# Kernel tuning notes

Measured on AMD Instinct MI355X. Metric: run time of the kernel, lower is better.

## Reference

```python
import jax, jax.numpy as jnp
import numpy as np

N = 100000        # nodes
E = 1_600_000     # edges (before self loops)
G = 512           # graphs in batch
IN = 64           # in_channels
HID = 48          # hidden_channels
H = 4             # heads
C = HID // H      # per-head channels
OUT = 10          # out_channels


def setup_inputs() -> dict:
    key = jax.random.key(0)
    ks = jax.random.split(key, 24)
    s = 0.1
    inp = {
        "x": jax.random.normal(ks[0], (N, IN), jnp.float32),
        "edge_index": jax.random.randint(ks[1], (2, E), 0, N, dtype=jnp.int64),
        "edge_weight": jax.random.uniform(ks[2], (E,), jnp.float32),
        "batch": jnp.sort(jax.random.randint(ks[3], (N,), 0, G, dtype=jnp.int64)),
        # GATConv layer 0 (IN -> H*C), layers 1,2 (HID -> H*C); bias=False
        "Wg0": jax.random.normal(ks[4], (IN, HID), jnp.float32) * s,
        "as0": jax.random.normal(ks[5], (H, C), jnp.float32) * s,
        "ad0": jax.random.normal(ks[6], (H, C), jnp.float32) * s,
        "Wg1": jax.random.normal(ks[7], (HID, HID), jnp.float32) * s,
        "as1": jax.random.normal(ks[8], (H, C), jnp.float32) * s,
        "ad1": jax.random.normal(ks[9], (H, C), jnp.float32) * s,
        "Wg2": jax.random.normal(ks[10], (HID, HID), jnp.float32) * s,
        "as2": jax.random.normal(ks[11], (H, C), jnp.float32) * s,
        "ad2": jax.random.normal(ks[12], (H, C), jnp.float32) * s,
        # MLP head: Linear(HID,HID) -> BatchNorm -> ReLU -> Linear(HID,OUT)
        "mW1": jax.random.normal(ks[13], (HID, HID), jnp.float32) * s,
        "mb1": jnp.zeros((HID,), jnp.float32),
        "gamma": jnp.ones((HID,), jnp.float32),
        "beta": jnp.zeros((HID,), jnp.float32),
        "mW2": jax.random.normal(ks[14], (HID, OUT), jnp.float32) * s,
        "mb2": jnp.zeros((OUT,), jnp.float32),
    }
    return inp


def _gat_layer(x, src, dst, W, a_src, a_dst):
    # x: [N, F_in] -> per-head features [N, H, C]
    xh = (x @ W).reshape(N, H, C)
    al_s = (xh * a_src).sum(-1)   # [N, H] source attention term
    al_d = (xh * a_dst).sum(-1)   # [N, H] target attention term
    logit = jax.nn.leaky_relu(al_s[src] + al_d[dst], negative_slope=0.2)  # [E', H]
    # segment softmax over incoming edges of each target node
    m = jax.ops.segment_max(logit, dst, num_segments=N)
    e = jnp.exp(logit - m[dst])
    denom = jax.ops.segment_sum(e, dst, num_segments=N)
    alpha = e / (denom[dst] + 1e-16)                     # [E', H]
    msg = xh[src] * alpha[:, :, None]                    # [E', H, C]
    out = jax.ops.segment_sum(msg, dst, num_segments=N)  # [N, H, C]
    return out.reshape(N, H * C)


def reference(x, edge_index, edge_weight, batch, Wg0, as0, ad0, Wg1, as1, ad1,
              Wg2, as2, ad2, mW1, mb1, gamma, beta, mW2, mb2):
    loops = jnp.arange(N, dtype=edge_index.dtype)
    src = jnp.concatenate([edge_index[0], loops])  # add_self_loops=True
    dst = jnp.concatenate([edge_index[1], loops])

    h = jax.nn.relu(_gat_layer(x, src, dst, Wg0, as0, ad0))
    h = jax.nn.relu(_gat_layer(h, src, dst, Wg1, as1, ad1))
    h = jax.nn.relu(_gat_layer(h, src, dst, Wg2, as2, ad2))

    # global mean pool over graph ids
    sums = jax.ops.segment_sum(h, batch, num_segments=G)
    cnt = jax.ops.segment_sum(jnp.ones((N,), h.dtype), batch, num_segments=G)
    g = sums / jnp.maximum(cnt, 1.0)[:, None]            # [G, HID]

    # MLP head (dropout = eval identity; BatchNorm with batch stats)
    z = g @ mW1 + mb1
    mu = z.mean(0)
    var = z.var(0)
    z = (z - mu) * jax.lax.rsqrt(var + 1e-5) * gamma + beta
    z = jax.nn.relu(z)
    last = z @ mW2 + mb2                                 # [G, OUT]

    logp = jax.nn.log_softmax(last, -1)
    soft = jax.nn.softmax(last, -1)  # softmax(log_softmax(x)) == softmax(x)
    return (logp, soft, last)
```

## Files before the change

kernel.cpp:

```cpp
#include <hip/hip_runtime.h>
#include <cstdint>

#define GRAPHS 512
#define HEADS 4
#define CPH 12
#define HID 48
#define NPAIR 24
#define RECW 32
#define OUTC 10
#define WPB 4
#define MAXBUCK 1024
#define BCAP 8192
#define BCHUNK 8192

__device__ __forceinline__ float bflo(unsigned u){ return __uint_as_float(u<<16); }
__device__ __forceinline__ float bfhi(unsigned u){ return __uint_as_float(u&0xFFFF0000u); }
__device__ __forceinline__ unsigned pack_bf16(float a, float b){
    unsigned ua=__float_as_uint(a), ub=__float_as_uint(b);
    ua += 0x7FFFu + ((ua>>16)&1u);
    ub += 0x7FFFu + ((ub>>16)&1u);
    return (ua>>16) | (ub & 0xFFFF0000u);
}

__device__ __forceinline__ void fma4(float4& a, const float4 h,
    const float4 w0, const float4 w1, const float4 w2, const float4 w3)
{
    a.x = fmaf(h.x, w0.x, a.x); a.x = fmaf(h.y, w1.x, a.x); a.x = fmaf(h.z, w2.x, a.x); a.x = fmaf(h.w, w3.x, a.x);
    a.y = fmaf(h.x, w0.y, a.y); a.y = fmaf(h.y, w1.y, a.y); a.y = fmaf(h.z, w2.y, a.y); a.y = fmaf(h.w, w3.y, a.y);
    a.z = fmaf(h.x, w0.z, a.z); a.z = fmaf(h.y, w1.z, a.z); a.z = fmaf(h.z, w2.z, a.z); a.z = fmaf(h.w, w3.z, a.z);
    a.w = fmaf(h.x, w0.w, a.w); a.w = fmaf(h.y, w1.w, a.w); a.w = fmaf(h.z, w2.w, a.w); a.w = fmaf(h.w, w3.w, a.w);
}

template<int FIN, bool BF16IN>
__global__ __launch_bounds__(192) void gemm_al_kernel(
    const void* __restrict__ hin_, const float* __restrict__ W,
    const float* __restrict__ avs, const float* __restrict__ avd,
    unsigned* __restrict__ rec, int n)
{
    const int NPB = 64;
    const int SHW = FIN / 4 + 1;
    __shared__ float4 sH[NPB * SHW];
    __shared__ float4 sW4[FIN * 12];
    __shared__ float sA[HID], sB[HID];
    __shared__ float sPS[NPB][13];
    __shared__ float sPD[NPB][13];

    const int t = threadIdx.x;
    const int base = blockIdx.x * NPB;

    for (int i = t; i < FIN * 12; i += 192) sW4[i] = ((const float4*)W)[i];
    if (t < HID) { sA[t] = avs[t]; sB[t] = avd[t]; }

    if (BF16IN) {
        const unsigned* hin = (const unsigned*)hin_;
        float* sHf = (float*)sH;
        const int RW = 4 * SHW;
        for (int i = t; i < NPB * (FIN / 2); i += 192) {
            int r = i / (FIN / 2), pc = i % (FIN / 2);
            int node = base + r;
            unsigned u = (node < n) ? hin[(size_t)node * (FIN / 2) + pc] : 0u;
            sHf[r * RW + 2 * pc]     = bflo(u);
            sHf[r * RW + 2 * pc + 1] = bfhi(u);
        }
    } else {
        const float4* hin = (const float4*)hin_;
        for (int i = t; i < NPB * (FIN / 4); i += 192) {
            int r = i / (FIN / 4), q = i % (FIN / 4);
            int node = base + r;
            sH[r * SHW + q] = (node < n) ? hin[(size_t)node * (FIN / 4) + q]
                                         : float4{0.f,0.f,0.f,0.f};
        }
    }
    __syncthreads();

    const int cs = t >> 4;
    const int ns = t & 15;

    float4 acc0{0.f,0.f,0.f,0.f}, acc1{0.f,0.f,0.f,0.f};
    float4 acc2{0.f,0.f,0.f,0.f}, acc3{0.f,0.f,0.f,0.f};

    #pragma unroll
    for (int kq = 0; kq < FIN / 4; ++kq) {
        float4 w0 = sW4[(4 * kq + 0) * 12 + cs];
        float4 w1 = sW4[(4 * kq + 1) * 12 + cs];
        float4 w2 = sW4[(4 * kq + 2) * 12 + cs];
        float4 w3 = sW4[(4 * kq + 3) * 12 + cs];
        float4 h0 = sH[(ns +  0) * SHW + kq];
        float4 h1 = sH[(ns + 16) * SHW + kq];
        float4 h2 = sH[(ns + 32) * SHW + kq];
        float4 h3 = sH[(ns + 48) * SHW + kq];
        fma4(acc0, h0, w0, w1, w2, w3);
        fma4(acc1, h1, w0, w1, w2, w3);
        fma4(acc2, h2, w0, w1, w2, w3);
        fma4(acc3, h3, w0, w1, w2, w3);
    }

    const float A0 = sA[4*cs], A1 = sA[4*cs+1], A2 = sA[4*cs+2], A3 = sA[4*cs+3];
    const float B0 = sB[4*cs], B1 = sB[4*cs+1], B2 = sB[4*cs+2], B3 = sB[4*cs+3];
    sPS[ns +  0][cs] = fmaf(acc0.x,A0, fmaf(acc0.y,A1, fmaf(acc0.z,A2, acc0.w*A3)));
    sPD[ns +  0][cs] = fmaf(acc0.x,B0, fmaf(acc0.y,B1, fmaf(acc0.z,B2, acc0.w*B3)));
    sPS[ns + 16][cs] = fmaf(acc1.x,A0, fmaf(acc1.y,A1, fmaf(acc1.z,A2, acc1.w*A3)));
    sPD[ns + 16][cs] = fmaf(acc1.x,B0, fmaf(acc1.y,B1, fmaf(acc1.z,B2, acc1.w*B3)));
    sPS[ns + 32][cs] = fmaf(acc2.x,A0, fmaf(acc2.y,A1, fmaf(acc2.z,A2, acc2.w*A3)));
    sPD[ns + 32][cs] = fmaf(acc2.x,B0, fmaf(acc2.y,B1, fmaf(acc2.z,B2, acc2.w*B3)));
    sPS[ns + 48][cs] = fmaf(acc3.x,A0, fmaf(acc3.y,A1, fmaf(acc3.z,A2, acc3.w*A3)));
    sPD[ns + 48][cs] = fmaf(acc3.x,B0, fmaf(acc3.y,B1, fmaf(acc3.z,B2, acc3.w*B3)));

    {
        int node = base + ns;
        if (node < n) {
            uint2* rp = (uint2*)(rec + (size_t)node * RECW + 4 + 2 * cs);
            *rp = uint2{pack_bf16(acc0.x, acc0.y), pack_bf16(acc0.z, acc0.w)};
        }
        node = base + ns + 16;
        if (node < n) {
            uint2* rp = (uint2*)(rec + (size_t)node * RECW + 4 + 2 * cs);
            *rp = uint2{pack_bf16(acc1.x, acc1.y), pack_bf16(acc1.z, acc1.w)};
        }
        node = base + ns + 32;
        if (node < n) {
            uint2* rp = (uint2*)(rec + (size_t)node * RECW + 4 + 2 * cs);
            *rp = uint2{pack_bf16(acc2.x, acc2.y), pack_bf16(acc2.z, acc2.w)};
        }
        node = base + ns + 48;
        if (node < n) {
            uint2* rp = (uint2*)(rec + (size_t)node * RECW + 4 + 2 * cs);
            *rp = uint2{pack_bf16(acc3.x, acc3.y), pack_bf16(acc3.z, acc3.w)};
        }
    }

    __syncthreads();
    if (t < NPB) {
        int node = base + t;
        if (node < n) {
            float4 als4, ald4;
            als4.x = sPS[t][0] + sPS[t][1]  + sPS[t][2];
            als4.y = sPS[t][3] + sPS[t][4]  + sPS[t][5];
            als4.z = sPS[t][6] + sPS[t][7]  + sPS[t][8];
            als4.w = sPS[t][9] + sPS[t][10] + sPS[t][11];
            ald4.x = sPD[t][0] + sPD[t][1]  + sPD[t][2];
            ald4.y = sPD[t][3] + sPD[t][4]  + sPD[t][5];
            ald4.z = sPD[t][6] + sPD[t][7]  + sPD[t][8];
            ald4.w = sPD[t][9] + sPD[t][10] + sPD[t][11];
            float* recf = (float*)(rec + (size_t)node * RECW);
            *(float4*)recf        = als4;
            *(float4*)(recf + 28) = ald4;
        }
    }
}

__global__ __launch_bounds__(256) void passAB_kernel(
    const int* __restrict__ esrc, const int* __restrict__ edst, int E,
    int* __restrict__ gcur, unsigned* __restrict__ ebuf, int nbuck)
{
    __shared__ int lcnt[MAXBUCK];
    __shared__ int lbase[MAXBUCK];
    for (int i = threadIdx.x; i < nbuck; i += 256) lcnt[i] = 0;
    __syncthreads();
    int e0 = blockIdx.x * BCHUNK, e1 = min(E, e0 + BCHUNK);
    for (int e = e0 + threadIdx.x; e < e1; e += 256)
        atomicAdd(&lcnt[edst[e] >> 8], 1);
    __syncthreads();
    for (int i = threadIdx.x; i < nbuck; i += 256) {
        int c = lcnt[i];
        lbase[i] = c ? (i * BCAP + atomicAdd(&gcur[i], c)) : 0;
        lcnt[i] = 0;
    }
    __syncthreads();
    for (int e = e0 + threadIdx.x; e < e1; e += 256) {
        int d = edst[e], s = esrc[e];
        int b = d >> 8;
        int rk = atomicAdd(&lcnt[b], 1);
        ebuf[lbase[b] + rk] = ((unsigned)(d & 255) << 24) | (unsigned)s;
    }
}

__global__ __launch_bounds__(1024) void bscan_kernel(
    const int* __restrict__ bcnt, int* __restrict__ boff, int nbuck, int etot)
{
    __shared__ int s[1024];
    int t = threadIdx.x;
    int v = (t < nbuck) ? bcnt[t] : 0;
    s[t] = v; __syncthreads();
    for (int off = 1; off < 1024; off <<= 1) {
        int a = (t >= off) ? s[t - off] : 0;
        __syncthreads();
        s[t] += a;
        __syncthreads();
    }
    if (t < nbuck) boff[t] = s[t] - v;
    if (t == 0) boff[nbuck] = etot;
}

__global__ __launch_bounds__(256) void passC_kernel(
    const unsigned* __restrict__ ebuf, const int* __restrict__ boff,
    const int* __restrict__ bcnt,
    int* __restrict__ rowptr, int* __restrict__ colidx, int n, int E)
{
    __shared__ int lcnt[256];
    __shared__ int sc[256];
    __shared__ int lcur[256];
    int b = blockIdx.x, t = threadIdx.x;
    int nbase = b << 8;
    lcnt[t] = 0;
    __syncthreads();
    int s0 = b * BCAP;
    int s1 = s0 + bcnt[b];
    for (int i = s0 + t; i < s1; i += 256)
        atomicAdd(&lcnt[ebuf[i] >> 24], 1);
    __syncthreads();
    sc[t] = lcnt[t]; __syncthreads();
    for (int off = 1; off < 256; off <<= 1) {
        int v = (t >= off) ? sc[t - off] : 0;
        __syncthreads();
        sc[t] += v;
        __syncthreads();
    }
    int rp = boff[b] + sc[t] - lcnt[t];
    if (nbase + t < n) rowptr[nbase + t] = rp;
    if (b == (int)gridDim.x - 1 && t == 0) rowptr[n] = E;
    lcur[t] = rp;
    __syncthreads();
    for (int i = s0 + t; i < s1; i += 256) {
        unsigned u = ebuf[i];
        int pos = atomicAdd(&lcur[u >> 24], 1);
        colidx[pos] = (int)(u & 0xFFFFFFu);
    }
}

__global__ __launch_bounds__(256) void agg_kernel(
    const int* __restrict__ rowptr, const int* __restrict__ colidx,
    const unsigned* __restrict__ rec,
    unsigned* __restrict__ hb, int n)
{
    __shared__ float tb[WPB][2][32][5];
    __shared__ int   sb[WPB][2][32];
    const int w = threadIdx.x >> 6, lane = threadIdx.x & 63;
    const int half = lane >> 5, l32 = lane & 31;
    const int node = (blockIdx.x * WPB + w) * 2 + half;
    const bool act = node < n;

    int start = 0, end = 0;
    if (act) { start = rowptr[node]; end = rowptr[node + 1]; }

    const unsigned* nrec = rec + (size_t)node * RECW;
    float4 asn  = act ? *(const float4*)(nrec)      : float4{0.f,0.f,0.f,0.f};
    float4 aldn = act ? *(const float4*)(nrec + 28) : float4{0.f,0.f,0.f,0.f};

    const bool fmaL = l32 < NPAIR;
    const int p  = fmaL ? l32 : 0;
    const int hh = p / 6;

    float tself;
    {
        float as_h = hh < 2 ? (hh == 0 ? asn.x : asn.y) : (hh == 2 ? asn.z : asn.w);
        float ad_h = hh < 2 ? (hh == 0 ? aldn.x : aldn.y) : (hh == 2 ? aldn.z : aldn.w);
        float ls = as_h + ad_h; ls = ls > 0.f ? ls : 0.2f * ls;
        tself = __expf(ls);
    }

    float a0 = 0.f, a1 = 0.f, a2 = 0.f, a3 = 0.f;
    float den = tself;
    if (act && fmaL) {
        unsigned u = nrec[4 + p];
        a0 = tself * bflo(u);
        a1 = tself * bfhi(u);
    }

    const char* recb = (const char*)rec;
    const int poff = 16 + 4 * p;

    if (start < end) {
        int idx = start + l32; if (idx >= end) idx = end - 1;
        int s_nx = colidx[idx];
        float4 al_nx = *(const float4*)(recb + ((size_t)(unsigned)s_nx << 7));

        for (int cb = start; cb < end; cb += 32) {
            const int m = min(32, end - cb);
            {
                sb[w][half][l32] = s_nx << 7;
                float l0 = al_nx.x + aldn.x; l0 = l0 > 0.f ? l0 : 0.2f * l0;
                float l1 = al_nx.y + aldn.y; l1 = l1 > 0.f ? l1 : 0.2f * l1;
                float l2 = al_nx.z + aldn.z; l2 = l2 > 0.f ? l2 : 0.2f * l2;
                float l3 = al_nx.w + aldn.w; l3 = l3 > 0.f ? l3 : 0.2f * l3;
                tb[w][half][l32][0] = __expf(l0);
                tb[w][half][l32][1] = __expf(l1);
                tb[w][half][l32][2] = __expf(l2);
                tb[w][half][l32][3] = __expf(l3);
            }
            const int cb2 = cb + 32;
            if (cb2 < end) {
                int idx2 = cb2 + l32; if (idx2 >= end) idx2 = end - 1;
                s_nx = colidx[idx2];
                al_nx = *(const float4*)(recb + ((size_t)(unsigned)s_nx << 7));
            }
            __builtin_amdgcn_sched_barrier(0);
            if (fmaL) {
                int j = 0;
                for (; j + 4 <= m; j += 4) {
                    int o0 = sb[w][half][j+0], o1 = sb[w][half][j+1];
                    int o2 = sb[w][half][j+2], o3 = sb[w][half][j+3];
                    float t0 = tb[w][half][j+0][hh], t1 = tb[w][half][j+1][hh];
                    float t2 = tb[w][half][j+2][hh], t3 = tb[w][half][j+3][hh];
                    unsigned u0 = *(const unsigned*)(recb + o0 + poff);
                    unsigned u1 = *(const unsigned*)(recb + o1 + poff);
                    unsigned u2 = *(const unsigned*)(recb + o2 + poff);
                    unsigned u3 = *(const unsigned*)(recb + o3 + poff);
                    den += (t0 + t1) + (t2 + t3);
                    a0 = fmaf(t0, bflo(u0), a0); a1 = fmaf(t0, bfhi(u0), a1);
                    a2 = fmaf(t1, bflo(u1), a2); a3 = fmaf(t1, bfhi(u1), a3);
                    a0 = fmaf(t2, bflo(u2), a0); a1 = fmaf(t2, bfhi(u2), a1);
                    a2 = fmaf(t3, bflo(u3), a2); a3 = fmaf(t3, bfhi(u3), a3);
                }
                for (; j < m; ++j) {
                    int o0 = sb[w][half][j];
                    float t0 = tb[w][half][j][hh];
                    unsigned u0 = *(const unsigned*)(recb + o0 + poff);
                    den += t0;
                    a0 = fmaf(t0, bflo(u0), a0); a1 = fmaf(t0, bfhi(u0), a1);
                }
            }
            __builtin_amdgcn_sched_barrier(0);
        }
    }

    if (act && fmaL) {
        float inv = 1.f / (den + 1e-16f);
        float vLo = (a0 + a2) * inv; vLo = vLo > 0.f ? vLo : 0.f;
        float vHi = (a1 + a3) * inv; vHi = vHi > 0.f ? vHi : 0.f;
        hb[(size_t)node * NPAIR + p] = pack_bf16(vLo, vHi);
    }
}

__global__ __launch_bounds__(256) void pool_mlp1_kernel(
    const unsigned* __restrict__ hb, const int* __restrict__ batch,
    const float* __restrict__ W1, const float* __restrict__ b1,
    float* __restrict__ z, int n)
{
    __shared__ float sLo[8][NPAIR];
    __shared__ float sHi[8][NPAIR];
    __shared__ float sg[HID];
    int g = blockIdx.x;
    int lo = 0, hi = n;
    while (lo < hi) { int mid = (lo + hi) >> 1; if (batch[mid] < g) lo = mid + 1; else hi = mid; }
    int start = lo;
    lo = start; hi = n;
    while (lo < hi) { int mid = (lo + hi) >> 1; if (batch[mid] < g + 1) lo = mid + 1; else hi = mid; }
    int end = lo;

    int r = threadIdx.x >> 5;
    int p = threadIdx.x & 31;
    if (p < NPAIR) {
        float aLo = 0.f, aHi = 0.f;
        for (int i = start + r; i < end; i += 8) {
            unsigned u = hb[(size_t)i * NPAIR + p];
            aLo += bflo(u); aHi += bfhi(u);
        }
        sLo[r][p] = aLo; sHi[r][p] = aHi;
    }
    __syncthreads();
    if (threadIdx.x < NPAIR) {
        float l = 0.f, h2 = 0.f;
        #pragma unroll
        for (int rr = 0; rr < 8; ++rr) { l += sLo[rr][threadIdx.x]; h2 += sHi[rr][threadIdx.x]; }
        float cnt = (float)(end > start ? end - start : 1);
        sg[2 * threadIdx.x]     = l / cnt;
        sg[2 * threadIdx.x + 1] = h2 / cnt;
    }
    __syncthreads();
    int c = threadIdx.x;
    if (c < HID) {
        float acc = b1[c];
        #pragma unroll
        for (int k = 0; k < HID; ++k) acc = fmaf(sg[k], W1[k * HID + c], acc);
        z[g * HID + c] = acc;
    }
}

__global__ __launch_bounds__(256) void bn_stats_kernel(
    const float* __restrict__ z, float* __restrict__ mu, float* __restrict__ rsig)
{
    int j = blockIdx.x;
    int t = threadIdx.x;
    float s = 0.f, s2 = 0.f;
    for (int i = t; i < GRAPHS; i += 256) {
        float v = z[i * HID + j];
        s += v; s2 += v * v;
    }
    __shared__ float rs[256], rs2[256];
    rs[t] = s; rs2[t] = s2; __syncthreads();
    for (int off = 128; off > 0; off >>= 1) {
        if (t < off) { rs[t] += rs[t + off]; rs2[t] += rs2[t + off]; }
        __syncthreads();
    }
    if (t == 0) {
        float m = rs[0] / GRAPHS;
        float var = rs2[0] / GRAPHS - m * m;
        mu[j] = m;
        rsig[j] = rsqrtf(var + 1e-5f);
    }
}

__global__ __launch_bounds__(64) void head_kernel(
    const float* __restrict__ z, const float* __restrict__ mu, const float* __restrict__ rsig,
    const float* __restrict__ gamma, const float* __restrict__ beta,
    const float* __restrict__ W2, const float* __restrict__ b2,
    float* __restrict__ out)
{
    __shared__ float zn[HID];
    __shared__ float lastv[OUTC];
    __shared__ float red[2];
    int g = blockIdx.x;
    int t = threadIdx.x;
    if (t < HID) {
        float v = (z[g * HID + t] - mu[t]) * rsig[t] * gamma[t] + beta[t];
        zn[t] = v > 0.f ? v : 0.f;
    }
    __syncthreads();
    if (t < OUTC) {
        float acc = b2[t];
        #pragma unroll
        for (int k = 0; k < HID; ++k) acc = fmaf(zn[k], W2[k * OUTC + t], acc);
        lastv[t] = acc;
    }
    __syncthreads();
    if (t == 0) {
        float m = lastv[0];
        for (int o = 1; o < OUTC; ++o) m = fmaxf(m, lastv[o]);
        float se = 0.f;
        for (int o = 0; o < OUTC; ++o) se += expf(lastv[o] - m);
        red[0] = m; red[1] = logf(se);
    }
    __syncthreads();
    if (t < OUTC) {
        float l = lastv[t];
        float lp = l - red[0] - red[1];
        out[g * OUTC + t] = lp;
        out[GRAPHS * OUTC + g * OUTC + t] = expf(lp);
        out[2 * GRAPHS * OUTC + g * OUTC + t] = l;
    }
}

extern "C" void kernel_launch(void* const* d_in, const int* in_sizes, int n_in,
                              void* d_out, int out_size, void* d_ws, size_t ws_size,
                              hipStream_t stream)
{
    const float* x     = (const float*)d_in[0];
    const int*   ei    = (const int*)  d_in[1];
    const int*   batch = (const int*)  d_in[3];
    const float* Wg0 = (const float*)d_in[4];
    const float* as0 = (const float*)d_in[5];
    const float* ad0 = (const float*)d_in[6];
    const float* Wg1 = (const float*)d_in[7];
    const float* as1 = (const float*)d_in[8];
    const float* ad1 = (const float*)d_in[9];
    const float* Wg2 = (const float*)d_in[10];
    const float* as2 = (const float*)d_in[11];
    const float* ad2 = (const float*)d_in[12];
    const float* mW1 = (const float*)d_in[13];
    const float* mb1 = (const float*)d_in[14];
    const float* gamma = (const float*)d_in[15];
    const float* beta  = (const float*)d_in[16];
    const float* mW2 = (const float*)d_in[17];
    const float* mb2 = (const float*)d_in[18];

    const int n  = in_sizes[3];
    const int E  = in_sizes[1] / 2;
    const int FIN0 = in_sizes[0] / n;
    const int nbuck = (n + 255) >> 8;

    unsigned* rec = (unsigned*)d_ws;
    unsigned* hb  = rec + (size_t)n * RECW;
    float* zbuf  = (float*)(hb + (size_t)n * NPAIR);
    float* mu    = zbuf + GRAPHS * HID;
    float* rsig  = mu + HID;
    int* rowptr  = (int*)(rsig + HID);
    int* boff    = rowptr + (n + 1);
    int* gcur    = boff + (MAXBUCK + 1);
    unsigned* ebuf = (unsigned*)(gcur + MAXBUCK);
    int* colidx  = (int*)(ebuf + (size_t)nbuck * BCAP);

    const int* esrc = ei;
    const int* edst = ei + E;

    hipMemsetAsync(gcur, 0, MAXBUCK * sizeof(int), stream);
    passAB_kernel<<<(E + BCHUNK - 1) / BCHUNK, 256, 0, stream>>>(esrc, edst, E, gcur, ebuf, nbuck);
    bscan_kernel<<<1, 1024, 0, stream>>>(gcur, boff, nbuck, E);
    passC_kernel<<<nbuck, 256, 0, stream>>>(ebuf, boff, gcur, rowptr, colidx, n, E);

    const int gemm_blocks = (n + 63) / 64;
    const int agg_blocks  = (n + 2 * WPB - 1) / (2 * WPB);

    if (FIN0 == 64)
        gemm_al_kernel<64, false><<<gemm_blocks, 192, 0, stream>>>(x, Wg0, as0, ad0, rec, n);
    else
        gemm_al_kernel<48, false><<<gemm_blocks, 192, 0, stream>>>(x, Wg0, as0, ad0, rec, n);
    agg_kernel<<<agg_blocks, 256, 0, stream>>>(rowptr, colidx, rec, hb, n);
    gemm_al_kernel<48, true><<<gemm_blocks, 192, 0, stream>>>(hb, Wg1, as1, ad1, rec, n);
    agg_kernel<<<agg_blocks, 256, 0, stream>>>(rowptr, colidx, rec, hb, n);
    gemm_al_kernel<48, true><<<gemm_blocks, 192, 0, stream>>>(hb, Wg2, as2, ad2, rec, n);
    agg_kernel<<<agg_blocks, 256, 0, stream>>>(rowptr, colidx, rec, hb, n);

    pool_mlp1_kernel<<<GRAPHS, 256, 0, stream>>>(hb, batch, mW1, mb1, zbuf, n);
    bn_stats_kernel<<<HID, 256, 0, stream>>>(zbuf, mu, rsig);
    head_kernel<<<GRAPHS, 64, 0, stream>>>(zbuf, mu, rsig, gamma, beta, mW2, mb2, (float*)d_out);
}
```

Baseline: 354.4 us.

## Enlarge GEMM node tile, cache dst in LDS, unroll aggregation by eight

Three independent changes. The GEMM kernel now handles 96 nodes per block instead of 64, with six accumulators per thread, so each weight load is reused more and fewer blocks are launched. The bucketing pass keeps the destination indices in shared memory so the second pass does not read them from global memory again. The aggregation inner loop gets an 8-wide unrolled path to issue more gathers in flight. These raise register and LDS use, which could lower occupancy.

```diff
diff --git a/kernel.cpp b/kernel.cpp
--- a/kernel.cpp
+++ b/kernel.cpp
@@ -37,7 +37,7 @@
     const float* __restrict__ avs, const float* __restrict__ avd,
     unsigned* __restrict__ rec, int n)
 {
-    const int NPB = 64;
+    const int NPB = 96;
     const int SHW = FIN / 4 + 1;
     __shared__ float4 sH[NPB * SHW];
     __shared__ float4 sW4[FIN * 12];
@@ -76,8 +76,8 @@
     const int cs = t >> 4;
     const int ns = t & 15;
 
-    float4 acc0{0.f,0.f,0.f,0.f}, acc1{0.f,0.f,0.f,0.f};
-    float4 acc2{0.f,0.f,0.f,0.f}, acc3{0.f,0.f,0.f,0.f};
+    float4 acc0{0.f,0.f,0.f,0.f}, acc1{0.f,0.f,0.f,0.f}, acc2{0.f,0.f,0.f,0.f};
+    float4 acc3{0.f,0.f,0.f,0.f}, acc4{0.f,0.f,0.f,0.f}, acc5{0.f,0.f,0.f,0.f};
 
     #pragma unroll
     for (int kq = 0; kq < FIN / 4; ++kq) {
@@ -89,10 +89,14 @@
         float4 h1 = sH[(ns + 16) * SHW + kq];
         float4 h2 = sH[(ns + 32) * SHW + kq];
         float4 h3 = sH[(ns + 48) * SHW + kq];
+        float4 h4 = sH[(ns + 64) * SHW + kq];
+        float4 h5 = sH[(ns + 80) * SHW + kq];
         fma4(acc0, h0, w0, w1, w2, w3);
         fma4(acc1, h1, w0, w1, w2, w3);
         fma4(acc2, h2, w0, w1, w2, w3);
         fma4(acc3, h3, w0, w1, w2, w3);
+        fma4(acc4, h4, w0, w1, w2, w3);
+        fma4(acc5, h5, w0, w1, w2, w3);
     }
 
     const float A0 = sA[4*cs], A1 = sA[4*cs+1], A2 = sA[4*cs+2], A3 = sA[4*cs+3];
@@ -105,6 +109,10 @@
     sPD[ns + 32][cs] = fmaf(acc2.x,B0, fmaf(acc2.y,B1, fmaf(acc2.z,B2, acc2.w*B3)));
     sPS[ns + 48][cs] = fmaf(acc3.x,A0, fmaf(acc3.y,A1, fmaf(acc3.z,A2, acc3.w*A3)));
     sPD[ns + 48][cs] = fmaf(acc3.x,B0, fmaf(acc3.y,B1, fmaf(acc3.z,B2, acc3.w*B3)));
+    sPS[ns + 64][cs] = fmaf(acc4.x,A0, fmaf(acc4.y,A1, fmaf(acc4.z,A2, acc4.w*A3)));
+    sPD[ns + 64][cs] = fmaf(acc4.x,B0, fmaf(acc4.y,B1, fmaf(acc4.z,B2, acc4.w*B3)));
+    sPS[ns + 80][cs] = fmaf(acc5.x,A0, fmaf(acc5.y,A1, fmaf(acc5.z,A2, acc5.w*A3)));
+    sPD[ns + 80][cs] = fmaf(acc5.x,B0, fmaf(acc5.y,B1, fmaf(acc5.z,B2, acc5.w*B3)));
 
     {
         int node = base + ns;
@@ -126,6 +134,16 @@
         if (node < n) {
             uint2* rp = (uint2*)(rec + (size_t)node * RECW + 4 + 2 * cs);
             *rp = uint2{pack_bf16(acc3.x, acc3.y), pack_bf16(acc3.z, acc3.w)};
+        }
+        node = base + ns + 64;
+        if (node < n) {
+            uint2* rp = (uint2*)(rec + (size_t)node * RECW + 4 + 2 * cs);
+            *rp = uint2{pack_bf16(acc4.x, acc4.y), pack_bf16(acc4.z, acc4.w)};
+        }
+        node = base + ns + 80;
+        if (node < n) {
+            uint2* rp = (uint2*)(rec + (size_t)node * RECW + 4 + 2 * cs);
+            *rp = uint2{pack_bf16(acc5.x, acc5.y), pack_bf16(acc5.z, acc5.w)};
         }
     }
 
@@ -155,11 +173,15 @@
 {
     __shared__ int lcnt[MAXBUCK];
     __shared__ int lbase[MAXBUCK];
+    __shared__ int sD[BCHUNK];
     for (int i = threadIdx.x; i < nbuck; i += 256) lcnt[i] = 0;
     __syncthreads();
     int e0 = blockIdx.x * BCHUNK, e1 = min(E, e0 + BCHUNK);
-    for (int e = e0 + threadIdx.x; e < e1; e += 256)
-        atomicAdd(&lcnt[edst[e] >> 8], 1);
+    for (int e = e0 + threadIdx.x; e < e1; e += 256) {
+        int d = edst[e];
+        sD[e - e0] = d;
+        atomicAdd(&lcnt[d >> 8], 1);
+    }
     __syncthreads();
     for (int i = threadIdx.x; i < nbuck; i += 256) {
         int c = lcnt[i];
@@ -168,7 +190,7 @@
     }
     __syncthreads();
     for (int e = e0 + threadIdx.x; e < e1; e += 256) {
-        int d = edst[e], s = esrc[e];
+        int d = sD[e - e0], s = esrc[e];
         int b = d >> 8;
         int rk = atomicAdd(&lcnt[b], 1);
         ebuf[lbase[b] + rk] = ((unsigned)(d & 255) << 24) | (unsigned)s;
@@ -297,6 +319,33 @@
             __builtin_amdgcn_sched_barrier(0);
             if (fmaL) {
                 int j = 0;
+                for (; j + 8 <= m; j += 8) {
+                    int o0 = sb[w][half][j+0], o1 = sb[w][half][j+1];
+                    int o2 = sb[w][half][j+2], o3 = sb[w][half][j+3];
+                    int o4 = sb[w][half][j+4], o5 = sb[w][half][j+5];
+                    int o6 = sb[w][half][j+6], o7 = sb[w][half][j+7];
+                    float t0 = tb[w][half][j+0][hh], t1 = tb[w][half][j+1][hh];
+                    float t2 = tb[w][half][j+2][hh], t3 = tb[w][half][j+3][hh];
+                    float t4 = tb[w][half][j+4][hh], t5 = tb[w][half][j+5][hh];
+                    float t6 = tb[w][half][j+6][hh], t7 = tb[w][half][j+7][hh];
+                    unsigned u0 = *(const unsigned*)(recb + o0 + poff);
+                    unsigned u1 = *(const unsigned*)(recb + o1 + poff);
+                    unsigned u2 = *(const unsigned*)(recb + o2 + poff);
+                    unsigned u3 = *(const unsigned*)(recb + o3 + poff);
+                    unsigned u4 = *(const unsigned*)(recb + o4 + poff);
+                    unsigned u5 = *(const unsigned*)(recb + o5 + poff);
+                    unsigned u6 = *(const unsigned*)(recb + o6 + poff);
+                    unsigned u7 = *(const unsigned*)(recb + o7 + poff);
+                    den += ((t0 + t1) + (t2 + t3)) + ((t4 + t5) + (t6 + t7));
+                    a0 = fmaf(t0, bflo(u0), a0); a1 = fmaf(t0, bfhi(u0), a1);
+                    a2 = fmaf(t1, bflo(u1), a2); a3 = fmaf(t1, bfhi(u1), a3);
+                    a0 = fmaf(t2, bflo(u2), a0); a1 = fmaf(t2, bfhi(u2), a1);
+                    a2 = fmaf(t3, bflo(u3), a2); a3 = fmaf(t3, bfhi(u3), a3);
+                    a0 = fmaf(t4, bflo(u4), a0); a1 = fmaf(t4, bfhi(u4), a1);
+                    a2 = fmaf(t5, bflo(u5), a2); a3 = fmaf(t5, bfhi(u5), a3);
+                    a0 = fmaf(t6, bflo(u6), a0); a1 = fmaf(t6, bfhi(u6), a1);
+                    a2 = fmaf(t7, bflo(u7), a2); a3 = fmaf(t7, bfhi(u7), a3);
+                }
                 for (; j + 4 <= m; j += 4) {
                     int o0 = sb[w][half][j+0], o1 = sb[w][half][j+1];
                     int o2 = sb[w][half][j+2], o3 = sb[w][half][j+3];
@@ -488,7 +537,7 @@
     bscan_kernel<<<1, 1024, 0, stream>>>(gcur, boff, nbuck, E);
     passC_kernel<<<nbuck, 256, 0, stream>>>(ebuf, boff, gcur, rowptr, colidx, n, E);
 
-    const int gemm_blocks = (n + 63) / 64;
+    const int gemm_blocks = (n + 95) / 96;
     const int agg_blocks  = (n + 2 * WPB - 1) / (2 * WPB);
 
     if (FIN0 == 64)
```

Result: no change. 355.7 us (+0.4%).
